# Kernel optimization log

Hardware: AMD Instinct MI355X
Metric: run time of the kernel (lower is better)

Reference implementation:

```python
import jax, jax.numpy as jnp
import numpy as np

B, P, H, A = 256, 196, 1024, 512

def setup_inputs() -> dict:
    key = jax.random.key(0)
    ks = jax.random.split(key, 20)
    s = 1.0 / np.sqrt(H)
    sa = 1.0 / np.sqrt(A)
    return {
        "spatial_image": jax.random.normal(ks[0], (B, P, H), jnp.float32),
        "decoder_out": jax.random.normal(ks[1], (B, H), jnp.float32),
        "st": jax.random.normal(ks[2], (B, H), jnp.float32),
        "W_sen_aff": jax.random.uniform(ks[3], (H, H), jnp.float32, -s, s),
        "b_sen_aff": jax.random.uniform(ks[4], (H,), jnp.float32, -s, s),
        "W_sen_att": jax.random.uniform(ks[5], (H, A), jnp.float32, -s, s),
        "b_sen_att": jax.random.uniform(ks[6], (A,), jnp.float32, -s, s),
        "W_h_aff": jax.random.uniform(ks[7], (H, H), jnp.float32, -s, s),
        "b_h_aff": jax.random.uniform(ks[8], (H,), jnp.float32, -s, s),
        "W_h_att": jax.random.uniform(ks[9], (H, A), jnp.float32, -s, s),
        "b_h_att": jax.random.uniform(ks[10], (A,), jnp.float32, -s, s),
        "W_v_att": jax.random.uniform(ks[11], (H, A), jnp.float32, -s, s),
        "b_v_att": jax.random.uniform(ks[12], (A,), jnp.float32, -s, s),
        "W_alpha": jax.random.uniform(ks[13], (A, 1), jnp.float32, -sa, sa),
        "b_alpha": jax.random.uniform(ks[14], (1,), jnp.float32, -sa, sa),
        "W_ctx": jax.random.uniform(ks[15], (H, H), jnp.float32, -s, s),
        "b_ctx": jax.random.uniform(ks[16], (H,), jnp.float32, -s, s),
    }

def reference(spatial_image, decoder_out, st,
              W_sen_aff, b_sen_aff, W_sen_att, b_sen_att,
              W_h_aff, b_h_aff, W_h_att, b_h_att,
              W_v_att, b_v_att, W_alpha, b_alpha, W_ctx, b_ctx):
    # visual_attn: [B, P, A]
    visual_attn = jnp.einsum('bph,ha->bpa', spatial_image, W_v_att) + b_v_att
    # sentinel path: [B, H] -> relu affine -> [B, A]
    sentinel_affine = jax.nn.relu(st @ W_sen_aff + b_sen_aff)
    sentinel_attn = sentinel_affine @ W_sen_att + b_sen_att
    # hidden path: [B, H] -> tanh affine -> [B, A]
    hidden_affine = jnp.tanh(decoder_out @ W_h_aff + b_h_aff)
    hidden_attn = hidden_affine @ W_h_att + b_h_att
    # concat sentinel as an extra "pixel": [B, P+1, H] and [B, P+1, A]
    concat_features = jnp.concatenate([spatial_image, sentinel_affine[:, None, :]], axis=1)
    attended_features = jnp.concatenate([visual_attn, sentinel_attn[:, None, :]], axis=1)
    attention = jnp.tanh(attended_features + hidden_attn[:, None, :])  # [B, P+1, A]
    alpha = (jnp.einsum('bpa,ao->bpo', attention, W_alpha) + b_alpha)[..., 0]  # [B, P+1]
    att_weights = jax.nn.softmax(alpha, axis=1)
    context = jnp.einsum('bph,bp->bh', concat_features, att_weights)  # [B, H]
    beta_value = att_weights[:, -1:]  # [B, 1]
    out_l = jnp.tanh((context + hidden_affine) @ W_ctx + b_ctx)  # [B, H]
    return (out_l, att_weights, beta_value)
```

## Files before the change

### kernel.cpp

```cpp
#include <hip/hip_runtime.h>
#include <stdint.h>
#include <stddef.h>

typedef __attribute__((ext_vector_type(4))) float f32x4;
typedef __attribute__((ext_vector_type(8))) short short8;

#define MROWS 50176


static __device__ __forceinline__ int lds_off(int row, int k) {
    int slot = (k >> 3) ^ ((row >> 1) & 3);
    return (row << 6) + (slot << 4) + ((k & 7) << 1);
}

static __device__ __forceinline__ unsigned div196(unsigned g) {
    return (unsigned)(((unsigned long long)g * 85599ull) >> 24);
}

static __device__ __forceinline__ unsigned short f2bf(float f) {
    union { float f; unsigned u; } v; v.f = f;
    unsigned r = v.u + 0x7FFFu + ((v.u >> 16) & 1u);
    return (unsigned short)(r >> 16);
}

static __device__ __forceinline__ unsigned long long pack4bf(f32x4 a) {
    return  (unsigned long long)f2bf(a[0])
         | ((unsigned long long)f2bf(a[1]) << 16)
         | ((unsigned long long)f2bf(a[2]) << 32)
         | ((unsigned long long)f2bf(a[3]) << 48);
}

static __device__ __forceinline__ float tanh_fast(float x) {
    float xc = fminf(fmaxf(x, -9.f), 9.f);
    float e = __builtin_amdgcn_exp2f(xc * 2.885390081777927f);
    return (e - 1.f) * __builtin_amdgcn_rcpf(e + 1.f);
}

static __device__ __forceinline__ void gload_lds16(const void* g, void* l) {
    __builtin_amdgcn_global_load_lds(
        (const __attribute__((address_space(1))) unsigned int*)g,
        (__attribute__((address_space(3))) unsigned int*)l, 16, 0, 0);
}

static __device__ __forceinline__ void kloop_dbuf(
    const float* __restrict__ Abase,
    const unsigned short* __restrict__ Bbase,
    char* sA0, char* sA1, char* sB0, char* sB1,
    f32x4 acc[4][4], int tid)
{
    const int lane = tid & 63, w = tid >> 6;
    const int lrow = lane & 15, lk = lane >> 4;
    const int wr = w >> 1, wc = w & 1;

    const float* Ap[4];
    int aoff[4];
    #pragma unroll
    for (int r = 0; r < 4; ++r) {
        int q = tid + (r << 8);
        int ar = q >> 3, kc = (q & 7) << 2;
        Ap[r] = Abase + (size_t)ar * 1024 + kc;
        aoff[r] = lds_off(ar, kc);
    }
    const unsigned short* Bp[2];
    int bdst[2];
    #pragma unroll
    for (int c = 0; c < 2; ++c) {
        int ch = (w << 1) + c;
        int row = (ch << 4) + (lane >> 2);
        int kg = (lane & 3) ^ ((row >> 1) & 3);
        Bp[c] = Bbase + (size_t)row * 1024 + (kg << 3);
        bdst[c] = ch << 10;
    }

    f32x4 z = {0.f, 0.f, 0.f, 0.f};
    #pragma unroll
    for (int m = 0; m < 4; ++m)
        #pragma unroll
        for (int n = 0; n < 4; ++n) acc[m][n] = z;

    {
        f32x4 a[4];
        #pragma unroll
        for (int r = 0; r < 4; ++r) a[r] = *(const f32x4*)Ap[r];
        #pragma unroll
        for (int c = 0; c < 2; ++c) gload_lds16(Bp[c], sB0 + bdst[c]);
        #pragma unroll
        for (int r = 0; r < 4; ++r)
            *(unsigned long long*)(sA0 + aoff[r]) = pack4bf(a[r]);
    }
    __syncthreads();

    char* sAc = sA0; char* sAn = sA1;
    char* sBc = sB0; char* sBn = sB1;
    for (int ks = 0; ks < 32; ++ks) {
        f32x4 an[4];
        if (ks < 31) {
            const int ko = (ks + 1) << 5;
            #pragma unroll
            for (int r = 0; r < 4; ++r) an[r] = *(const f32x4*)(Ap[r] + ko);
            #pragma unroll
            for (int c = 0; c < 2; ++c) gload_lds16(Bp[c] + ko, sBn + bdst[c]);
        }
        short8 af[4], bf[4];
        #pragma unroll
        for (int m = 0; m < 4; ++m)
            af[m] = *(const short8*)(sAc + lds_off((wr << 6) + (m << 4) + lrow, lk << 3));
        #pragma unroll
        for (int n = 0; n < 4; ++n)
            bf[n] = *(const short8*)(sBc + lds_off((wc << 6) + (n << 4) + lrow, lk << 3));
        #pragma unroll
        for (int m = 0; m < 4; ++m)
            #pragma unroll
            for (int n = 0; n < 4; ++n)
                acc[m][n] = __builtin_amdgcn_mfma_f32_16x16x32_bf16(af[m], bf[n], acc[m][n], 0, 0, 0);
        if (ks < 31) {
            #pragma unroll
            for (int r = 0; r < 4; ++r)
                *(unsigned long long*)(sAn + aoff[r]) = pack4bf(an[r]);
        }
        __syncthreads();
        char* t;
        t = sAc; sAc = sAn; sAn = t;
        t = sBc; sBc = sBn; sBn = t;
    }
}

__global__ __launch_bounds__(256, 4) void attn_alpha_kernel(
    const float* __restrict__ spatial,
    const unsigned short* __restrict__ WvT,
    const float* __restrict__ b_v_att,
    const float* __restrict__ hidden_attn,
    const float* __restrict__ W_alpha,
    float* __restrict__ alphap)
{
    __shared__ char sA[2][8192];
    __shared__ char sB[2][8192];
    __shared__ float alpha_s[128];
    const int tid = threadIdx.x;
    const int n4 = blockIdx.x & 3, mt = blockIdx.x >> 2;
    const int row0 = mt << 7, col0 = n4 << 7;
    if (tid < 128) alpha_s[tid] = 0.f;

    f32x4 acc[4][4];
    kloop_dbuf(spatial + (size_t)row0 * 1024, WvT + (size_t)col0 * 1024,
               sA[0], sA[1], sB[0], sB[1], acc, tid);

    const int lane = tid & 63, w = tid >> 6;
    const int wr = w >> 1, wc = w & 1;
    const int lrow = lane & 15, lk = lane >> 4;

    const unsigned bb0 = div196((unsigned)row0);
    const unsigned bb1 = div196((unsigned)(row0 + 127));
    float bv[4], wa[4], h0[4], h1[4];
    #pragma unroll
    for (int n = 0; n < 4; ++n) {
        int g = col0 + (wc << 6) + (n << 4) + lrow;
        bv[n] = b_v_att[g];
        wa[n] = W_alpha[g];
        h0[n] = hidden_attn[bb0 * 512 + g];
        h1[n] = hidden_attn[bb1 * 512 + g];
    }
    #pragma unroll
    for (int m = 0; m < 4; ++m) {
        #pragma unroll
        for (int i = 0; i < 4; ++i) {
            int rloc = (wr << 6) + (m << 4) + (lk << 2) + i;
            bool first = (div196((unsigned)(row0 + rloc)) == bb0);
            float s = 0.f;
            #pragma unroll
            for (int n = 0; n < 4; ++n) {
                float v = tanh_fast(acc[m][n][i] + bv[n] + (first ? h0[n] : h1[n]));
                s += v * wa[n];
            }
            #pragma unroll
            for (int off = 1; off < 16; off <<= 1) s += __shfl_xor(s, off);
            if (lrow == 0) atomicAdd(&alpha_s[rloc], s);
        }
    }
    __syncthreads();
    if (tid < 128)
        alphap[(size_t)n4 * MROWS + row0 + tid] = alpha_s[tid];
}

struct GemmDesc { const float* A; const unsigned short* BT; const float* bias; float* C; int N; int act; };
struct GemmPair { GemmDesc d[2]; };

__global__ __launch_bounds__(256, 4) void gemm_pair_kernel(GemmPair p)
{
    GemmDesc d = p.d[blockIdx.z];
    __shared__ char sA[2][8192];
    __shared__ char sB[2][8192];
    const int tid = threadIdx.x;
    const int row0 = blockIdx.x << 7;
    const int col0 = blockIdx.y << 7;
    f32x4 acc[4][4];
    kloop_dbuf(d.A + (size_t)row0 * 1024, d.BT + (size_t)col0 * 1024,
               sA[0], sA[1], sB[0], sB[1], acc, tid);
    const int lane = tid & 63, w = tid >> 6;
    const int wr = w >> 1, wc = w & 1;
    const int lrow = lane & 15, lk = lane >> 4;
    #pragma unroll
    for (int n = 0; n < 4; ++n) {
        int col = col0 + (wc << 6) + (n << 4) + lrow;
        float bs = d.bias[col];
        #pragma unroll
        for (int m = 0; m < 4; ++m) {
            int rbase = row0 + (wr << 6) + (m << 4) + (lk << 2);
            #pragma unroll
            for (int i = 0; i < 4; ++i) {
                float v = acc[m][n][i] + bs;
                if (d.act == 1) v = fmaxf(v, 0.f);
                if (d.act == 2) v = tanh_fast(v);
                d.C[(size_t)(rbase + i) * d.N + col] = v;
            }
        }
    }
}

struct TransDesc { const float* src; unsigned short* dst; int K; int N; };
struct TransArgs { TransDesc d[6]; };

__global__ void transpose_cvt_kernel(TransArgs args) {
    TransDesc d = args.d[blockIdx.y];
    int nt = d.N >> 5;
    int tiles = (d.K >> 5) * nt;
    if ((int)blockIdx.x >= tiles) return;
    int tk = blockIdx.x / nt, tn = blockIdx.x % nt;
    __shared__ unsigned short tile[32][33];
    int tx = threadIdx.x & 31, ty = threadIdx.x >> 5;
    int k0 = tk << 5, n0 = tn << 5;
    #pragma unroll
    for (int j = 0; j < 4; ++j)
        tile[ty + j * 8][tx] = f2bf(d.src[(size_t)(k0 + ty + j * 8) * d.N + n0 + tx]);
    __syncthreads();
    #pragma unroll
    for (int j = 0; j < 4; ++j)
        d.dst[(size_t)(n0 + ty + j * 8) * d.K + k0 + tx] = tile[tx][ty + j * 8];
}

__global__ void softmax_sentinel_kernel(
    const float* __restrict__ alphap,
    const float* __restrict__ sen_att, const float* __restrict__ hid_att,
    const float* __restrict__ W_alpha,
    float* __restrict__ att, float* __restrict__ beta)
{
    int b = blockIdx.x, tid = threadIdx.x;
    __shared__ float al[197];
    __shared__ float red[4];
    if (tid < 196) {
        size_t g = (size_t)b * 196 + tid;
        al[tid] = alphap[g] + alphap[MROWS + g] + alphap[2 * MROWS + g] + alphap[3 * MROWS + g];
    }
    float s = 0.f;
    for (int a = tid; a < 512; a += 256)
        s += tanh_fast(sen_att[b * 512 + a] + hid_att[b * 512 + a]) * W_alpha[a];
    #pragma unroll
    for (int off = 1; off < 64; off <<= 1) s += __shfl_xor(s, off);
    if ((tid & 63) == 0) red[tid >> 6] = s;
    __syncthreads();
    if (tid == 0) al[196] = red[0] + red[1] + red[2] + red[3];
    __syncthreads();
    if (tid < 64) {
        float v[4];
        float mx = -1e30f;
        #pragma unroll
        for (int j = 0; j < 4; ++j) {
            int i = tid + j * 64;
            v[j] = (i < 197) ? al[i] : -1e30f;
            mx = fmaxf(mx, v[j]);
        }
        #pragma unroll
        for (int off = 1; off < 64; off <<= 1) mx = fmaxf(mx, __shfl_xor(mx, off));
        float sm = 0.f;
        #pragma unroll
        for (int j = 0; j < 4; ++j) {
            v[j] = __builtin_amdgcn_exp2f((v[j] - mx) * 1.442695040888963f);
            if (tid + j * 64 >= 197) v[j] = 0.f;
            sm += v[j];
        }
        #pragma unroll
        for (int off = 1; off < 64; off <<= 1) sm += __shfl_xor(sm, off);
        float inv = 1.f / sm;
        #pragma unroll
        for (int j = 0; j < 4; ++j) {
            int i = tid + j * 64;
            if (i < 197) {
                float wv = v[j] * inv;
                att[b * 197 + i] = wv;
                if (i == 196) beta[b] = wv;
            }
        }
    }
}

__global__ __launch_bounds__(256) void context_kernel(
    const float* __restrict__ spatial, const float* __restrict__ sen_aff,
    const float* __restrict__ hid_aff, const float* __restrict__ att,
    float* __restrict__ ctxh)
{
    int b = blockIdx.x, half = blockIdx.y, t = threadIdx.x;
    __shared__ float wsm[197];
    if (t < 197) wsm[t] = att[b * 197 + t];
    __syncthreads();
    int h2 = (half << 8) + t;
    const float2* sp = (const float2*)(spatial + (size_t)b * 196 * 1024) + h2;
    float ax = 0.f, ay = 0.f;
    #pragma unroll 4
    for (int p = 0; p < 196; ++p) {
        float2 x = sp[(size_t)p * 512];
        ax += wsm[p] * x.x; ay += wsm[p] * x.y;
    }
    float w196 = wsm[196];
    float2 sa = ((const float2*)(sen_aff + (size_t)b * 1024))[h2];
    float2 ha = ((const float2*)(hid_aff + (size_t)b * 1024))[h2];
    ctxh[(size_t)b * 1024 + 2 * h2]     = ax + w196 * sa.x + ha.x;
    ctxh[(size_t)b * 1024 + 2 * h2 + 1] = ay + w196 * sa.y + ha.y;
}

extern "C" void kernel_launch(void* const* d_in, const int* in_sizes, int n_in,
                              void* d_out, int out_size, void* d_ws, size_t ws_size,
                              hipStream_t stream)
{
    const float* spatial   = (const float*)d_in[0];
    const float* decoder   = (const float*)d_in[1];
    const float* st        = (const float*)d_in[2];
    const float* W_sen_aff = (const float*)d_in[3];
    const float* b_sen_aff = (const float*)d_in[4];
    const float* W_sen_att = (const float*)d_in[5];
    const float* b_sen_att = (const float*)d_in[6];
    const float* W_h_aff   = (const float*)d_in[7];
    const float* b_h_aff   = (const float*)d_in[8];
    const float* W_h_att   = (const float*)d_in[9];
    const float* b_h_att   = (const float*)d_in[10];
    const float* W_v_att   = (const float*)d_in[11];
    const float* b_v_att   = (const float*)d_in[12];
    const float* W_alpha   = (const float*)d_in[13];
    const float* W_ctx     = (const float*)d_in[15];
    const float* b_ctx     = (const float*)d_in[16];

    char* ws = (char*)d_ws;
    size_t off = 0;
    auto alloc = [&](size_t bytes) {
        char* p = ws + off; off += (bytes + 255) & ~(size_t)255; return p;
    };
    unsigned short* WvT  = (unsigned short*)alloc((size_t)512 * 1024 * 2);
    unsigned short* WsaT = (unsigned short*)alloc((size_t)1024 * 1024 * 2);
    unsigned short* WstT = (unsigned short*)alloc((size_t)512 * 1024 * 2);
    unsigned short* WhaT = (unsigned short*)alloc((size_t)1024 * 1024 * 2);
    unsigned short* WhtT = (unsigned short*)alloc((size_t)512 * 1024 * 2);
    unsigned short* WcxT = (unsigned short*)alloc((size_t)1024 * 1024 * 2);
    float* sen_aff = (float*)alloc((size_t)256 * 1024 * 4);
    float* sen_att = (float*)alloc((size_t)256 * 512 * 4);
    float* hid_aff = (float*)alloc((size_t)256 * 1024 * 4);
    float* hid_att = (float*)alloc((size_t)256 * 512 * 4);
    float* alphap  = (float*)alloc((size_t)4 * MROWS * 4);
    float* ctxh    = (float*)alloc((size_t)256 * 1024 * 4);

    float* out_l    = (float*)d_out;
    float* out_att  = out_l + 256 * 1024;
    float* out_beta = out_att + 256 * 197;

    TransArgs ta;
    ta.d[0] = { W_v_att,   WvT,  1024, 512  };
    ta.d[1] = { W_sen_aff, WsaT, 1024, 1024 };
    ta.d[2] = { W_sen_att, WstT, 1024, 512  };
    ta.d[3] = { W_h_aff,   WhaT, 1024, 1024 };
    ta.d[4] = { W_h_att,   WhtT, 1024, 512  };
    ta.d[5] = { W_ctx,     WcxT, 1024, 1024 };
    transpose_cvt_kernel<<<dim3(1024, 6), 256, 0, stream>>>(ta);

    GemmPair p1;
    p1.d[0] = { st,      WsaT, b_sen_aff, sen_aff, 1024, 1 };
    p1.d[1] = { decoder, WhaT, b_h_aff,   hid_aff, 1024, 2 };
    gemm_pair_kernel<<<dim3(2, 8, 2), 256, 0, stream>>>(p1);

    GemmPair p2;
    p2.d[0] = { sen_aff, WstT, b_sen_att, sen_att, 512, 0 };
    p2.d[1] = { hid_aff, WhtT, b_h_att,   hid_att, 512, 0 };
    gemm_pair_kernel<<<dim3(2, 4, 2), 256, 0, stream>>>(p2);

    attn_alpha_kernel<<<1568, 256, 0, stream>>>(spatial, WvT, b_v_att, hid_att, W_alpha, alphap);
    softmax_sentinel_kernel<<<256, 256, 0, stream>>>(alphap, sen_att, hid_att, W_alpha, out_att, out_beta);
    context_kernel<<<dim3(256, 2), 256, 0, stream>>>(spatial, sen_aff, hid_aff, out_att, ctxh);

    GemmPair p3;
    p3.d[0] = { ctxh, WcxT, b_ctx, out_l, 1024, 2 };
    p3.d[1] = { ctxh, WcxT, b_ctx, out_l, 1024, 2 };
    gemm_pair_kernel<<<dim3(2, 8, 1), 256, 0, stream>>>(p3);
}
```

Baseline: 248.2 us.

## Remap attn block order, drop LDS atomics, use packed bf16 convert

The alpha kernel's block index is now remapped so that consecutive blocks are spread across groups of 8, and each block still covers one of the 392 M tiles times 4 N tiles. This is likely meant to help XCD/L2 locality. The shared-memory atomicAdd reduction is replaced with per-warp-column slots that are summed at the end, which removes the atomics and the zero-initialisation. The bf16 packing now uses the HIP packed float2-to-bf16 intrinsic, and the context loop unroll factor is raised from 4 to 8. Together these touch scheduling, synchronisation and instruction count, and some loop variables are renamed to avoid shadowing.

```diff
diff --git a/kernel.cpp b/kernel.cpp
--- a/kernel.cpp
+++ b/kernel.cpp
@@ -1,4 +1,5 @@
 #include <hip/hip_runtime.h>
+#include <hip/hip_bf16.h>
 #include <stdint.h>
 #include <stddef.h>
 
@@ -24,10 +25,10 @@
 }
 
 static __device__ __forceinline__ unsigned long long pack4bf(f32x4 a) {
-    return  (unsigned long long)f2bf(a[0])
-         | ((unsigned long long)f2bf(a[1]) << 16)
-         | ((unsigned long long)f2bf(a[2]) << 32)
-         | ((unsigned long long)f2bf(a[3]) << 48);
+    union { unsigned long long u; __hip_bfloat162 h[2]; } r;
+    r.h[0] = __float22bfloat162_rn(make_float2(a[0], a[1]));
+    r.h[1] = __float22bfloat162_rn(make_float2(a[2], a[3]));
+    return r.u;
 }
 
 static __device__ __forceinline__ float tanh_fast(float x) {
@@ -135,11 +136,12 @@
 {
     __shared__ char sA[2][8192];
     __shared__ char sB[2][8192];
-    __shared__ float alpha_s[128];
+    __shared__ float alpha_s[2][128];
     const int tid = threadIdx.x;
-    const int n4 = blockIdx.x & 3, mt = blockIdx.x >> 2;
+    const int j = blockIdx.x;
+    const int wk = (j & 7) * 196 + (j >> 3);
+    const int mt = wk >> 2, n4 = wk & 3;
     const int row0 = mt << 7, col0 = n4 << 7;
-    if (tid < 128) alpha_s[tid] = 0.f;
 
     f32x4 acc[4][4];
     kloop_dbuf(spatial + (size_t)row0 * 1024, WvT + (size_t)col0 * 1024,
@@ -174,12 +176,12 @@
             }
             #pragma unroll
             for (int off = 1; off < 16; off <<= 1) s += __shfl_xor(s, off);
-            if (lrow == 0) atomicAdd(&alpha_s[rloc], s);
+            if (lrow == 0) alpha_s[wc][rloc] = s;
         }
     }
     __syncthreads();
     if (tid < 128)
-        alphap[(size_t)n4 * MROWS + row0 + tid] = alpha_s[tid];
+        alphap[(size_t)n4 * MROWS + row0 + tid] = alpha_s[0][tid] + alpha_s[1][tid];
 }
 
 struct GemmDesc { const float* A; const unsigned short* BT; const float* bias; float* C; int N; int act; };
@@ -264,28 +266,28 @@
         float v[4];
         float mx = -1e30f;
         #pragma unroll
-        for (int j = 0; j < 4; ++j) {
-            int i = tid + j * 64;
-            v[j] = (i < 197) ? al[i] : -1e30f;
-            mx = fmaxf(mx, v[j]);
+        for (int jj = 0; jj < 4; ++jj) {
+            int i = tid + jj * 64;
+            v[jj] = (i < 197) ? al[i] : -1e30f;
+            mx = fmaxf(mx, v[jj]);
         }
         #pragma unroll
         for (int off = 1; off < 64; off <<= 1) mx = fmaxf(mx, __shfl_xor(mx, off));
         float sm = 0.f;
         #pragma unroll
-        for (int j = 0; j < 4; ++j) {
-            v[j] = __builtin_amdgcn_exp2f((v[j] - mx) * 1.442695040888963f);
-            if (tid + j * 64 >= 197) v[j] = 0.f;
-            sm += v[j];
+        for (int jj = 0; jj < 4; ++jj) {
+            v[jj] = __builtin_amdgcn_exp2f((v[jj] - mx) * 1.442695040888963f);
+            if (tid + jj * 64 >= 197) v[jj] = 0.f;
+            sm += v[jj];
         }
         #pragma unroll
         for (int off = 1; off < 64; off <<= 1) sm += __shfl_xor(sm, off);
         float inv = 1.f / sm;
         #pragma unroll
-        for (int j = 0; j < 4; ++j) {
-            int i = tid + j * 64;
+        for (int jj = 0; jj < 4; ++jj) {
+            int i = tid + jj * 64;
             if (i < 197) {
-                float wv = v[j] * inv;
+                float wv = v[jj] * inv;
                 att[b * 197 + i] = wv;
                 if (i == 196) beta[b] = wv;
             }
@@ -305,7 +307,7 @@
     int h2 = (half << 8) + t;
     const float2* sp = (const float2*)(spatial + (size_t)b * 196 * 1024) + h2;
     float ax = 0.f, ay = 0.f;
-    #pragma unroll 4
+    #pragma unroll 8
     for (int p = 0; p < 196; ++p) {
         float2 x = sp[(size_t)p * 512];
         ax += wsm[p] * x.x; ay += wsm[p] * x.y;
```

Measured after the change: 217.1 us. 1.14x faster.
